# Kernel optimization log

Measured on AMD Instinct MI355X. Metric: run time of the kernel, lower is better.

Reference implementation:

```python
import jax, jax.numpy as jnp
import numpy as np

B, TP, TF = 256, 128, 64
COV, D, OUT, CTRL, H, L = 64, 64, 32, 128, 512, 2


def _gru_layer(x, Wih, Whh, bih, bhh):
    # x: [B, T, in]; torch GRU gate order: r, z, n
    xg = jnp.einsum('bti,gi->btg', x, Wih) + bih  # [B, T, 3H]
    h0 = jnp.zeros((x.shape[0], Whh.shape[1]), x.dtype)

    def step(h, xg_t):
        gh = h @ Whh.T + bhh
        xr, xz, xn = jnp.split(xg_t, 3, axis=-1)
        hr, hz, hn = jnp.split(gh, 3, axis=-1)
        r = jax.nn.sigmoid(xr + hr)
        z = jax.nn.sigmoid(xz + hz)
        n = jnp.tanh(xn + r * hn)
        h = (1.0 - z) * n + z * h
        return h, h

    _, hs = jax.lax.scan(step, h0, jnp.swapaxes(xg, 0, 1))
    return jnp.swapaxes(hs, 0, 1)  # [B, T, H]


def setup_inputs() -> dict:
    key = jax.random.key(0)
    ks = jax.random.split(key, 32)
    s = 0.05
    inp = {
        'past_input': jax.random.normal(ks[0], (B, TP, COV), jnp.float32),
        'past_label': jax.random.normal(ks[1], (B, TP, OUT), jnp.float32),
        'future_input': jax.random.normal(ks[2], (B, TF, COV), jnp.float32),
        'gru_Wih_0': s * jax.random.normal(ks[3], (3 * H, COV), jnp.float32),
        'gru_Whh_0': s * jax.random.normal(ks[4], (3 * H, H), jnp.float32),
        'gru_bih_0': s * jax.random.normal(ks[5], (3 * H,), jnp.float32),
        'gru_bhh_0': s * jax.random.normal(ks[6], (3 * H,), jnp.float32),
        'gru_Wih_1': s * jax.random.normal(ks[7], (3 * H, H), jnp.float32),
        'gru_Whh_1': s * jax.random.normal(ks[8], (3 * H, H), jnp.float32),
        'gru_bih_1': s * jax.random.normal(ks[9], (3 * H,), jnp.float32),
        'gru_bhh_1': s * jax.random.normal(ks[10], (3 * H,), jnp.float32),
        'flow_u': s * jax.random.normal(ks[11], (D,), jnp.float32),
        'flow_w': s * jax.random.normal(ks[12], (D,), jnp.float32),
        'flow_b': s * jax.random.normal(ks[13], (D,), jnp.float32),
        'feat_W': s * jax.random.normal(ks[14], (D, H), jnp.float32),
        'feat_b': s * jax.random.normal(ks[15], (D,), jnp.float32),
        'ctrl_W1': s * jax.random.normal(ks[16], (CTRL, OUT), jnp.float32),
        'ctrl_b1': s * jax.random.normal(ks[17], (CTRL,), jnp.float32),
        'ctrl_W2': s * jax.random.normal(ks[18], (2 * D, CTRL), jnp.float32),
        'ctrl_b2': s * jax.random.normal(ks[19], (2 * D,), jnp.float32),
        'ctrlmu_W': s * jax.random.normal(ks[20], (D, D), jnp.float32),
        'ctrlmu_b': s * jax.random.normal(ks[21], (D,), jnp.float32),
        'out_W': s * jax.random.normal(ks[22], (OUT, D), jnp.float32),
        'out_b': s * jax.random.normal(ks[23], (OUT,), jnp.float32),
    }
    return inp


def reference(past_input, past_label, future_input,
              gru_Wih_0, gru_Whh_0, gru_bih_0, gru_bhh_0,
              gru_Wih_1, gru_Whh_1, gru_bih_1, gru_bhh_1,
              flow_u, flow_w, flow_b, feat_W, feat_b,
              ctrl_W1, ctrl_b1, ctrl_W2, ctrl_b2,
              ctrlmu_W, ctrlmu_b, out_W, out_b):
    cov = jnp.concatenate([past_input, future_input], axis=1)  # [B, T, COV]
    h1 = _gru_layer(cov, gru_Wih_0, gru_Whh_0, gru_bih_0, gru_bhh_0)
    cov_feat = _gru_layer(h1, gru_Wih_1, gru_Whh_1, gru_bih_1, gru_bhh_1)  # [B, T, H]
    Tp = past_input.shape[1]
    bsz = past_input.shape[0]

    def trans(mu_past, var_past, cov_t):
        # per-dim PlanarFlow vectorized over transition_dim
        a = jnp.tanh(flow_w * mu_past + flow_b)
        mu_prior = flow_u * a + cov_t @ feat_W.T + feat_b + mu_past
        coef = flow_u * flow_w * (1.0 - a * a)
        var_prior = 2.0 * coef * var_past + var_past + 1.0
        return mu_prior, var_prior

    def control(ctrl_in, mu_prior):
        hdn = jnp.tanh(ctrl_in @ ctrl_W1.T + ctrl_b1)
        cm, cls = jnp.split(hdn @ ctrl_W2.T + ctrl_b2, 2, axis=-1)
        cm = cm - (mu_prior @ ctrlmu_W.T + ctrlmu_b)
        return cm, jax.nn.softplus(cls)

    def fuse(mu_pr, var_pr, mu_po, var_po):
        s = var_po + var_pr
        mu_w = (var_po / s) * mu_pr + (var_pr / s) * mu_po
        return mu_w, var_pr * var_po / s

    def past_step(carry, xs):
        mu_post, var_post = carry
        cov_t, lab_t = xs
        mu_pr, var_pr = trans(mu_post, var_post, cov_t)
        pred = mu_pr @ out_W.T + out_b
        cm, cs = control(lab_t, mu_pr)
        return fuse(mu_pr, var_pr, cm, cs), (pred, cm, cs)

    def fut_step(carry, cov_t):
        mu_post, var_post = carry
        mu_pr, var_pr = trans(mu_post, var_post, cov_t)
        pred = mu_pr @ out_W.T + out_b
        cm, cs = control(pred, mu_pr)
        return fuse(mu_pr, var_pr, cm, cs), (pred, cm, cs)

    init = (jnp.zeros((bsz, D), cov.dtype), jnp.ones((bsz, D), cov.dtype))
    cov_p = jnp.swapaxes(cov_feat[:, :Tp], 0, 1)
    lab_p = jnp.swapaxes(past_label, 0, 1)
    carry, (pp, cmp_, csp) = jax.lax.scan(past_step, init, (cov_p, lab_p))
    cov_f = jnp.swapaxes(cov_feat[:, Tp:], 0, 1)
    _, (pf, cmf, csf) = jax.lax.scan(fut_step, carry, cov_f)

    pred = jnp.swapaxes(jnp.concatenate([pp, pf], axis=0), 0, 1)        # [B, T, OUT]
    cm = jnp.swapaxes(jnp.concatenate([cmp_, cmf], axis=0), 0, 1)[:, 1:]  # [B, T-1, D]
    cs = jnp.swapaxes(jnp.concatenate([csp, csf], axis=0), 0, 1)[:, 1:]   # [B, T-1, D]
    return pred, cm, cs
```

## Files before the change

kernel.cpp:

```cpp
#include <hip/hip_runtime.h>
#include <stdint.h>

#define DEV static __device__ __forceinline__

using short8 = __attribute__((ext_vector_type(8))) short;
using f32x4  = __attribute__((ext_vector_type(4))) float;
using gbl_u32 = const __attribute__((address_space(1))) unsigned int;
using lds_u32 = __attribute__((address_space(3))) unsigned int;

DEV float bf2f(short s) {
  unsigned u = ((unsigned)(unsigned short)s) << 16;
  float f; __builtin_memcpy(&f, &u, 4); return f;
}
DEV short f2bf(float f) {
  unsigned u; __builtin_memcpy(&u, &f, 4);
  u = (u + 0x7fffu + ((u >> 16) & 1u)) >> 16;
  return (short)u;
}
DEV void gload_lds16(const void* g, void* l) {
  __builtin_amdgcn_global_load_lds((gbl_u32*)g, (lds_u32*)l, 16, 0, 0);
}
DEV float sigm(float x) { return 1.f / (1.f + __expf(-x)); }
DEV float tanh_f(float x) {
  float e = __expf(2.f * x);
  return 1.f - 2.f * __builtin_amdgcn_rcpf(e + 1.f);
}
DEV void bar() {
  asm volatile("s_waitcnt lgkmcnt(0)" ::: "memory");
  __builtin_amdgcn_sched_barrier(0);
  __builtin_amdgcn_s_barrier();
  __builtin_amdgcn_sched_barrier(0);
}

__global__ void pack_cov_k(const float* __restrict__ past, const float* __restrict__ fut,
                           short* __restrict__ covp) {
  const int n = 192 * 256 * 64;
  for (int i = blockIdx.x * blockDim.x + threadIdx.x; i < n; i += gridDim.x * blockDim.x) {
    int c = i & 63, r = i >> 6;
    int b = r & 255, t = r >> 8;
    float v = (t < 128) ? past[((size_t)b * 128 + t) * 64 + c]
                        : fut[((size_t)b * 64 + (t - 128)) * 64 + c];
    covp[i] = f2bf(v);
  }
}

__global__ void pack_lab_k(const float* __restrict__ lab, short* __restrict__ labp) {
  const int n = 128 * 256 * 32;
  for (int i = blockIdx.x * blockDim.x + threadIdx.x; i < n; i += gridDim.x * blockDim.x) {
    int c = i & 31, r = i >> 5;
    int b = r & 255, t = r >> 8;
    labp[i] = f2bf(lab[((size_t)b * 128 + t) * 32 + c]);
  }
}

DEV int gru_srcrow(int pr) {
  int j = pr / 96, w = pr % 96;
  return ((w >> 5) << 9) + j * 32 + (w & 31);
}

__global__ void pack_gru_k(const float* __restrict__ Wih, const float* __restrict__ Whh,
                           const float* __restrict__ bih, const float* __restrict__ bhh,
                           int Kin, short* __restrict__ Wihp, short* __restrict__ Whhp,
                           float* __restrict__ bihp, float* __restrict__ bhhp) {
  const int nW1 = 1536 * Kin, nW2 = 1536 * 512;
  const int total = nW1 + nW2 + 3072;
  for (int idx = blockIdx.x * blockDim.x + threadIdx.x; idx < total; idx += gridDim.x * blockDim.x) {
    if (idx < nW1) {
      int pr = idx / Kin, k = idx - pr * Kin;
      Wihp[idx] = f2bf(Wih[(size_t)gru_srcrow(pr) * Kin + k]);
    } else if (idx < nW1 + nW2) {
      int ii = idx - nW1;
      int j = ii / 49152, r = ii - j * 49152;
      int i = r & 7, slot = r >> 3;
      int l = slot & 63, sf = slot >> 6;
      int kqg = sf / 6, tile = sf - kqg * 6;
      int w = tile * 16 + (l & 15);
      int k = kqg * 32 + (l >> 4) * 8 + i;
      int srow = (w >> 5) * 512 + j * 32 + (w & 31);
      Whhp[ii] = f2bf(Whh[(size_t)srow * 512 + k]);
    } else if (idx < nW1 + nW2 + 1536) {
      int pr = idx - nW1 - nW2;
      bihp[pr] = bih[gru_srcrow(pr)];
    } else {
      int pr = idx - nW1 - nW2 - 1536;
      bhhp[pr] = bhh[gru_srcrow(pr)];
    }
  }
}

__global__ void pack_misc_k(const float* __restrict__ fw, const float* __restrict__ w1,
                            const float* __restrict__ w2, short* __restrict__ fwb,
                            short* __restrict__ w1b, short* __restrict__ w2b) {
  const int n1 = 64 * 512, n2 = 128 * 32, n3 = 128 * 128;
  const int total = n1 + n2 + n3;
  for (int i = blockIdx.x * blockDim.x + threadIdx.x; i < total; i += gridDim.x * blockDim.x) {
    if (i < n1) fwb[i] = f2bf(fw[i]);
    else if (i < n1 + n2) w1b[i - n1] = f2bf(w1[i - n1]);
    else w2b[i - n1 - n2] = f2bf(w2[i - n1 - n2]);
  }
}

__global__ void pack_vae_k(const float* __restrict__ outW, const float* __restrict__ cmuW,
                           const float* __restrict__ W1, const float* __restrict__ W2,
                           short* __restrict__ vwf) {
  const int n = 52 * 512;
  for (int i = blockIdx.x * blockDim.x + threadIdx.x; i < n; i += gridDim.x * blockDim.x) {
    int fr = i >> 9, l = (i >> 3) & 63, e = i & 7;
    int lm = l & 15, lh = l >> 4;
    float v;
    if (fr < 4) { int kt = fr >> 1, nt = fr & 1; v = outW[(nt * 16 + lm) * 64 + kt * 32 + lh * 8 + e]; }
    else if (fr < 12) { int f = fr - 4, kt = f >> 2, nt = f & 3; v = cmuW[(nt * 16 + lm) * 64 + kt * 32 + lh * 8 + e]; }
    else if (fr < 20) { int nt = fr - 12; v = W1[(nt * 16 + lm) * 32 + lh * 8 + e]; }
    else { int f = fr - 20, kt = f >> 3, nt = f & 7; v = W2[(nt * 16 + lm) * 128 + kt * 32 + lh * 8 + e]; }
    vwf[i] = f2bf(v);
  }
}

template <int BK, bool OBF16, bool DOTANH, bool AFRAG, int CMODE = 0>
__global__ __launch_bounds__(256) void gemm_bt_k(
    const short* __restrict__ A, const short* __restrict__ Bw,
    const float* __restrict__ bias, void* __restrict__ Cout,
    int M, int N, int K) {
  constexpr int BM = 128, BN = 128;
  __shared__ short As[BM * BK];
  __shared__ short Bs[BN * BK];
  const int tid = threadIdx.x, lane = tid & 63;
  const int wave = tid >> 6, wm = wave >> 1, wn = wave & 1;
  const int bm = blockIdx.x, bn = blockIdx.y;
  const int lm = lane & 15, lk = (lane >> 4) * 8;
  f32x4 acc[4][4] = {};
  for (int k0 = 0; k0 < K; k0 += BK) {
    constexpr int BYTES = BM * BK * 2;
#pragma unroll
    for (int it = 0; it < BYTES / 4096; ++it) {
      int o = it * 4096 + tid * 16;
      if (AFRAG) {
        int sub = o >> 10, gl = sub >> 1, kk2 = sub & 1, inb = o & 1023;
        size_t region = ((size_t)(bm >> 1) * 16 + (bm & 1) * 8 + gl) * 16 + (k0 >> 5) + kk2;
        gload_lds16((const char*)A + region * 1024 + inb, (char*)As + (o - lane * 16));
      } else {
        int row = o / (BK * 2);
        int col = o - row * (BK * 2);
        const char* srcA = (const char*)A + (((size_t)(bm * BM + row)) * K + k0) * 2 + col;
        gload_lds16(srcA, (char*)As + (o - lane * 16));
      }
      int row = o / (BK * 2);
      int col = o - row * (BK * 2);
      int rb = bn * BN + row;
      if (rb >= N) rb = N - 1;
      const char* srcB = (const char*)Bw + (((size_t)rb) * K + k0) * 2 + col;
      gload_lds16(srcB, (char*)Bs + (o - lane * 16));
    }
    __syncthreads();
#pragma unroll
    for (int kk = 0; kk < BK / 32; ++kk) {
      short8 av[4], bv[4];
#pragma unroll
      for (int i = 0; i < 4; ++i) {
        if (AFRAG)
          av[i] = *(const short8*)((const char*)As + (((wm * 4 + i) * 2 + kk) << 10) + lane * 16);
        else
          av[i] = *(const short8*)((const char*)As + ((wm * 64 + i * 16 + lm) * BK + kk * 32 + lk) * 2);
      }
#pragma unroll
      for (int jv = 0; jv < 4; ++jv)
        bv[jv] = *(const short8*)((const char*)Bs + ((wn * 64 + jv * 16 + lm) * BK + kk * 32 + lk) * 2);
#pragma unroll
      for (int i = 0; i < 4; ++i)
#pragma unroll
        for (int jv = 0; jv < 4; ++jv)
          acc[i][jv] = __builtin_amdgcn_mfma_f32_16x16x32_bf16(av[i], bv[jv], acc[i][jv], 0, 0, 0);
    }
    __syncthreads();
  }
  if (CMODE == 1) {
    const int NT = N >> 4;
#pragma unroll
    for (int jv = 0; jv < 4; ++jv) {
      int col = bn * BN + wn * 64 + jv * 16 + lm;
      if (col >= N) continue;
      float bvl = bias[col];
#pragma unroll
      for (int i = 0; i < 4; ++i) {
        int rowblk = bm * 8 + wm * 4 + i;
        f32x4 v = acc[i][jv];
        v[0] += bvl; v[1] += bvl; v[2] += bvl; v[3] += bvl;
        *(f32x4*)((float*)Cout + (((size_t)rowblk * NT + (col >> 4)) << 8) + lane * 4) = v;
      }
    }
  } else {
#pragma unroll
    for (int jv = 0; jv < 4; ++jv) {
      int col = bn * BN + wn * 64 + jv * 16 + lm;
      if (col >= N) continue;
      float bvl = bias[col];
#pragma unroll
      for (int i = 0; i < 4; ++i) {
        int row0 = bm * BM + wm * 64 + i * 16 + (lane >> 4) * 4;
#pragma unroll
        for (int r = 0; r < 4; ++r) {
          float v = acc[i][jv][r] + bvl;
          if (DOTANH) v = tanhf(v);
          size_t off = (size_t)(row0 + r) * N + col;
          if (OBF16) ((short*)Cout)[off] = f2bf(v);
          else ((float*)Cout)[off] = v;
        }
      }
    }
  }
}

template <int SCHEME>
__global__ __launch_bounds__(256) void gru_scan_k(
    const short* __restrict__ xg, const short* __restrict__ Whhp,
    const float* __restrict__ bhhp, short* __restrict__ hbuf,
    unsigned int* __restrict__ ctr, unsigned int* __restrict__ flags, int t0) {
  __shared__ short Wl[96 * 512];
  __shared__ short hs[16 * 512];
  __shared__ float sc[2][16 * 101];
  __shared__ float bhs[96];
  const int tid = threadIdx.x, lane = tid & 63, wave = tid >> 6;
  const int x = blockIdx.x;
  const int g = (x & 7) + ((x >> 7) << 3);
  const int j = (x >> 3) & 15;
  unsigned int* __restrict__ myctr = ctr + g * 64;
  unsigned int* __restrict__ myflags = flags + g * 16;
  unsigned int* __restrict__ hbuf32 = (unsigned int*)hbuf;
  {
    const char* wsrc = (const char*)Whhp + (size_t)j * 98304;
#pragma unroll 4
    for (int it = 0; it < 24; ++it) {
      int o = it * 4096 + tid * 16;
      gload_lds16(wsrc + o, (char*)Wl + (o - lane * 16));
    }
    if (tid < 96) bhs[tid] = bhhp[j * 96 + tid];
  }
  const int wk = wave >> 1, wn3 = wave & 1;
  const int m = tid >> 4, up = tid & 15, u0 = up * 2;
  for (int tl = 0; tl < 48; ++tl) {
    const int t = t0 + tl;
    const char* hsrc = (const char*)hbuf + ((size_t)t * 16 + g) * 16384;
#pragma unroll
    for (int it = 0; it < 4; ++it) {
      int o = it * 4096 + tid * 16;
      gload_lds16(hsrc + o, (char*)hs + (o - lane * 16));
    }
    const unsigned int* xp = (const unsigned int*)(xg + ((size_t)tl * 256 + g * 16 + m) * 1536 + j * 96);
    unsigned int xr2 = xp[up], xz2 = xp[16 + up], xn2 = xp[32 + up];
    __syncthreads();
    f32x4 a3[3] = {};
#pragma unroll
    for (int kq = 0; kq < 8; ++kq) {
      int kqg = wk * 8 + kq;
      short8 av = *(const short8*)((const char*)hs + (kqg << 10) + lane * 16);
#pragma unroll
      for (int n = 0; n < 3; ++n) {
        short8 bv = *(const short8*)((const char*)Wl + ((kqg * 6 + wn3 * 3 + n) << 10) + lane * 16);
        a3[n] = __builtin_amdgcn_mfma_f32_16x16x32_bf16(av, bv, a3[n], 0, 0, 0);
      }
    }
#pragma unroll
    for (int n = 0; n < 3; ++n)
#pragma unroll
      for (int rr = 0; rr < 4; ++rr)
        sc[wk][((lane >> 4) * 4 + rr) * 101 + (wn3 * 3 + n) * 16 + (lane & 15)] = a3[n][rr];
    __syncthreads();
    {
      float Sr0 = sc[0][m * 101 + u0] + sc[1][m * 101 + u0];
      float Sr1 = sc[0][m * 101 + u0 + 1] + sc[1][m * 101 + u0 + 1];
      float Sz0 = sc[0][m * 101 + 32 + u0] + sc[1][m * 101 + 32 + u0];
      float Sz1 = sc[0][m * 101 + 33 + u0] + sc[1][m * 101 + 33 + u0];
      float Sn0 = sc[0][m * 101 + 64 + u0] + sc[1][m * 101 + 64 + u0];
      float Sn1 = sc[0][m * 101 + 65 + u0] + sc[1][m * 101 + 65 + u0];
      int hpa = ((j * 64 + (up >> 2) * 16 + m) << 4) + ((u0 & 7) << 1);
      unsigned int hpu = *(const unsigned int*)((const char*)hs + hpa);
      float hp0 = bf2f((short)(hpu & 0xffff)), hp1 = bf2f((short)(hpu >> 16));
      float r0 = sigm(bf2f((short)(xr2 & 0xffff)) + Sr0 + bhs[u0]);
      float r1 = sigm(bf2f((short)(xr2 >> 16)) + Sr1 + bhs[u0 + 1]);
      float z0 = sigm(bf2f((short)(xz2 & 0xffff)) + Sz0 + bhs[32 + u0]);
      float z1 = sigm(bf2f((short)(xz2 >> 16)) + Sz1 + bhs[33 + u0]);
      float n0 = tanhf(bf2f((short)(xn2 & 0xffff)) + r0 * (Sn0 + bhs[64 + u0]));
      float n1 = tanhf(bf2f((short)(xn2 >> 16)) + r1 * (Sn1 + bhs[65 + u0]));
      float h0 = (1.f - z0) * n0 + z0 * hp0;
      float h1 = (1.f - z1) * n1 + z1 * hp1;
      unsigned int hv = (unsigned int)(unsigned short)f2bf(h0) |
                        ((unsigned int)(unsigned short)f2bf(h1) << 16);
      size_t oi = ((size_t)(t + 1) * 16 + g) * 4096 +
                  (j * 64 + (up >> 2) * 16 + m) * 4 + (up & 3);
      __hip_atomic_store(hbuf32 + oi, hv, __ATOMIC_RELAXED, __HIP_MEMORY_SCOPE_AGENT);
    }
    __syncthreads();
    if constexpr (SCHEME == 1) {
      if (tid == 0) {
        __hip_atomic_fetch_add(myctr, 1u, __ATOMIC_RELAXED, __HIP_MEMORY_SCOPE_AGENT);
        const unsigned tgt = 16u * (unsigned)(tl + 1);
        int guard = 0;
        while (__hip_atomic_load(myctr, __ATOMIC_RELAXED, __HIP_MEMORY_SCOPE_AGENT) < tgt &&
               ++guard < 200000) {}
      }
    } else {
      const unsigned tgt = (unsigned)(tl + 1);
      if (tid == 0)
        __hip_atomic_store(myflags + j, tgt, __ATOMIC_RELAXED, __HIP_MEMORY_SCOPE_AGENT);
      if (tid < 16) {
        int guard = 0;
        while (__hip_atomic_load(myflags + tid, __ATOMIC_RELAXED, __HIP_MEMORY_SCOPE_AGENT) < tgt &&
               ++guard < 200000) {}
      }
    }
    __syncthreads();
  }
}

#define PAST_STEP(T, FN, CMR, CSR)                                           \
  do {                                                                       \
    f32x4 muPr, varPr;                                                       \
    _Pragma("unroll") for (int r = 0; r < 4; ++r) {                          \
      float m_ = muC[r];                                                     \
      float a_ = tanh_f(fw1 * m_ + fb1);                                     \
      muPr[r] = fu1 * a_ + FN[r] + m_;                                       \
      float cf_ = fu1 * fw1 * (1.f - a_ * a_);                               \
      varPr[r] = 2.f * cf_ * varC[r] + varC[r] + 1.f;                        \
    }                                                                        \
    f32x4 cmNow = CMR, csNow = CSR;                                          \
    FN = *(const f32x4*)(feat_img + (((size_t)((T) + 2) * 16 + bg) * 4 + w) * 256 + l * 4); \
    if ((T) + 2 < 128) {                                                     \
      CMR = *(const f32x4*)(ctrl_img + (((size_t)((T) + 2) * 16 + bg) * 8 + w) * 256 + l * 4); \
      CSR = *(const f32x4*)(ctrl_img + (((size_t)((T) + 2) * 16 + bg) * 8 + 4 + w) * 256 + l * 4); \
    }                                                                        \
    _Pragma("unroll") for (int r = 0; r < 4; ++r) {                          \
      int row_ = m4 * 4 + r;                                                 \
      *(short*)((char*)muA + ((row_ * 128 + (w * 16 + c) * 2) ^ ((row_ & 7) << 4))) = f2bf(muPr[r]); \
    }                                                                        \
    bar();                                                                   \
    short8 muAf0 = *(const short8*)((const char*)muA + ((c * 128 + m4 * 16) ^ ((c & 7) << 4))); \
    short8 muAf1 = *(const short8*)((const char*)muA + ((c * 128 + 64 + m4 * 16) ^ ((c & 7) << 4))); \
    if (w == 0) *(short8*)(muprb + (((size_t)(T) * 16 + bg) * 2) * 512 + l * 8) = muAf0; \
    if (w == 1) *(short8*)(muprb + (((size_t)(T) * 16 + bg) * 2 + 1) * 512 + l * 8) = muAf1; \
    f32x4 mcC = {0.f, 0.f, 0.f, 0.f};                                        \
    mcC = __builtin_amdgcn_mfma_f32_16x16x32_bf16(muAf0, cmuf0, mcC, 0, 0, 0); \
    mcC = __builtin_amdgcn_mfma_f32_16x16x32_bf16(muAf1, cmuf1, mcC, 0, 0, 0); \
    bar();                                                                   \
    _Pragma("unroll") for (int r = 0; r < 4; ++r) {                          \
      float vp_ = varPr[r], mp_ = muPr[r];                                   \
      float cmv_ = cmNow[r] - (mcC[r] + cmub1);                              \
      float x_ = csNow[r];                                                   \
      float cs_ = (x_ > 20.f) ? x_ : __logf(1.f + __expf(x_));               \
      if ((T) >= 1) {                                                        \
        size_t b_ = (size_t)(bg * 16 + m4 * 4 + r);                          \
        out[1572864 + b_ * 12224 + (size_t)((T) - 1) * 64 + w * 16 + c] = cmv_; \
        out[4702208 + b_ * 12224 + (size_t)((T) - 1) * 64 + w * 16 + c] = cs_;  \
      }                                                                      \
      float s_ = cs_ + vp_;                                                  \
      float rs_ = __builtin_amdgcn_rcpf(s_);                                 \
      muC[r] = cs_ * rs_ * mp_ + vp_ * rs_ * cmv_;                           \
      varC[r] = vp_ * cs_ * rs_;                                             \
    }                                                                        \
  } while (0)

#define FUT_STEP(T, FN)                                                      \
  do {                                                                       \
    f32x4 muPr, varPr;                                                       \
    _Pragma("unroll") for (int r = 0; r < 4; ++r) {                          \
      float m_ = muC[r];                                                     \
      float a_ = tanh_f(fw1 * m_ + fb1);                                     \
      muPr[r] = fu1 * a_ + FN[r] + m_;                                       \
      float cf_ = fu1 * fw1 * (1.f - a_ * a_);                               \
      varPr[r] = 2.f * cf_ * varC[r] + varC[r] + 1.f;                        \
    }                                                                        \
    if ((T) + 2 < 192)                                                       \
      FN = *(const f32x4*)(feat_img + (((size_t)((T) + 2) * 16 + bg) * 4 + w) * 256 + l * 4); \
    _Pragma("unroll") for (int r = 0; r < 4; ++r) {                          \
      int row_ = m4 * 4 + r;                                                 \
      *(short*)((char*)muA + ((row_ * 128 + (w * 16 + c) * 2) ^ ((row_ & 7) << 4))) = f2bf(muPr[r]); \
    }                                                                        \
    bar();                                                                   \
    short8 muAf0 = *(const short8*)((const char*)muA + ((c * 128 + m4 * 16) ^ ((c & 7) << 4))); \
    short8 muAf1 = *(const short8*)((const char*)muA + ((c * 128 + 64 + m4 * 16) ^ ((c & 7) << 4))); \
    f32x4 mcC = {0.f, 0.f, 0.f, 0.f};                                        \
    mcC = __builtin_amdgcn_mfma_f32_16x16x32_bf16(muAf0, cmuf0, mcC, 0, 0, 0); \
    mcC = __builtin_amdgcn_mfma_f32_16x16x32_bf16(muAf1, cmuf1, mcC, 0, 0, 0); \
    if (w < 2) {                                                             \
      f32x4 predC = {0.f, 0.f, 0.f, 0.f};                                    \
      predC = __builtin_amdgcn_mfma_f32_16x16x32_bf16(muAf0, outWf0, predC, 0, 0, 0); \
      predC = __builtin_amdgcn_mfma_f32_16x16x32_bf16(muAf1, outWf1, predC, 0, 0, 0); \
      _Pragma("unroll") for (int r = 0; r < 4; ++r) {                        \
        float pv_ = predC[r] + outb1;                                        \
        out[(size_t)(bg * 16 + m4 * 4 + r) * 6144 + (T) * 32 + w * 16 + c] = pv_; \
        int row_ = m4 * 4 + r;                                               \
        *(short*)((char*)predA + ((row_ * 64 + (w * 16 + c) * 2) ^ ((row_ & 3) << 4))) = f2bf(pv_); \
      }                                                                      \
    }                                                                        \
    bar();                                                                   \
    short8 pAf = *(const short8*)((const char*)predA + ((c * 64 + m4 * 16) ^ ((c & 3) << 4))); \
    f32x4 z0 = {0.f, 0.f, 0.f, 0.f}, z1 = {0.f, 0.f, 0.f, 0.f};              \
    z0 = __builtin_amdgcn_mfma_f32_16x16x32_bf16(pAf, *(const short8*)((const char*)Wctl + (2 * w) * 1024 + l * 16), z0, 0, 0, 0); \
    z1 = __builtin_amdgcn_mfma_f32_16x16x32_bf16(pAf, *(const short8*)((const char*)Wctl + (2 * w + 1) * 1024 + l * 16), z1, 0, 0, 0); \
    _Pragma("unroll") for (int r = 0; r < 4; ++r) {                          \
      int row_ = m4 * 4 + r;                                                 \
      *(short*)((char*)hdnA + ((row_ * 256 + ((2 * w) * 16 + c) * 2) ^ ((row_ & 7) << 4))) = f2bf(tanh_f(z0[r] + b1a)); \
      *(short*)((char*)hdnA + ((row_ * 256 + ((2 * w + 1) * 16 + c) * 2) ^ ((row_ & 7) << 4))) = f2bf(tanh_f(z1[r] + b1b)); \
    }                                                                        \
    bar();                                                                   \
    short8 hAf0 = *(const short8*)((const char*)hdnA + ((c * 256 + 0 * 64 + m4 * 16) ^ ((c & 7) << 4))); \
    short8 hAf1 = *(const short8*)((const char*)hdnA + ((c * 256 + 1 * 64 + m4 * 16) ^ ((c & 7) << 4))); \
    short8 hAf2 = *(const short8*)((const char*)hdnA + ((c * 256 + 2 * 64 + m4 * 16) ^ ((c & 7) << 4))); \
    short8 hAf3 = *(const short8*)((const char*)hdnA + ((c * 256 + 3 * 64 + m4 * 16) ^ ((c & 7) << 4))); \
    f32x4 zcm = {0.f, 0.f, 0.f, 0.f}, zcs = {0.f, 0.f, 0.f, 0.f};            \
    zcm = __builtin_amdgcn_mfma_f32_16x16x32_bf16(hAf0, *(const short8*)((const char*)Wctl + (8 + 0 * 8 + w) * 1024 + l * 16), zcm, 0, 0, 0); \
    zcm = __builtin_amdgcn_mfma_f32_16x16x32_bf16(hAf1, *(const short8*)((const char*)Wctl + (8 + 1 * 8 + w) * 1024 + l * 16), zcm, 0, 0, 0); \
    zcm = __builtin_amdgcn_mfma_f32_16x16x32_bf16(hAf2, *(const short8*)((const char*)Wctl + (8 + 2 * 8 + w) * 1024 + l * 16), zcm, 0, 0, 0); \
    zcm = __builtin_amdgcn_mfma_f32_16x16x32_bf16(hAf3, *(const short8*)((const char*)Wctl + (8 + 3 * 8 + w) * 1024 + l * 16), zcm, 0, 0, 0); \
    zcs = __builtin_amdgcn_mfma_f32_16x16x32_bf16(hAf0, *(const short8*)((const char*)Wctl + (8 + 0 * 8 + 4 + w) * 1024 + l * 16), zcs, 0, 0, 0); \
    zcs = __builtin_amdgcn_mfma_f32_16x16x32_bf16(hAf1, *(const short8*)((const char*)Wctl + (8 + 1 * 8 + 4 + w) * 1024 + l * 16), zcs, 0, 0, 0); \
    zcs = __builtin_amdgcn_mfma_f32_16x16x32_bf16(hAf2, *(const short8*)((const char*)Wctl + (8 + 2 * 8 + 4 + w) * 1024 + l * 16), zcs, 0, 0, 0); \
    zcs = __builtin_amdgcn_mfma_f32_16x16x32_bf16(hAf3, *(const short8*)((const char*)Wctl + (8 + 3 * 8 + 4 + w) * 1024 + l * 16), zcs, 0, 0, 0); \
    bar();                                                                   \
    _Pragma("unroll") for (int r = 0; r < 4; ++r) {                          \
      float vp_ = varPr[r], mp_ = muPr[r];                                   \
      float cmv_ = (zcm[r] + b2cm) - (mcC[r] + cmub1);                       \
      float x_ = zcs[r] + b2cs;                                              \
      float cs_ = (x_ > 20.f) ? x_ : __logf(1.f + __expf(x_));               \
      size_t b_ = (size_t)(bg * 16 + m4 * 4 + r);                            \
      out[1572864 + b_ * 12224 + (size_t)((T) - 1) * 64 + w * 16 + c] = cmv_; \
      out[4702208 + b_ * 12224 + (size_t)((T) - 1) * 64 + w * 16 + c] = cs_;  \
      float s_ = cs_ + vp_;                                                  \
      float rs_ = __builtin_amdgcn_rcpf(s_);                                 \
      muC[r] = cs_ * rs_ * mp_ + vp_ * rs_ * cmv_;                           \
      varC[r] = vp_ * cs_ * rs_;                                             \
    }                                                                        \
  } while (0)

__global__ __launch_bounds__(256) void vae_k(
    const float* __restrict__ feat_img, const float* __restrict__ ctrl_img,
    const short* __restrict__ vwf,
    const float* __restrict__ flow_u, const float* __restrict__ flow_w,
    const float* __restrict__ flow_b, const float* __restrict__ outb,
    const float* __restrict__ b1, const float* __restrict__ b2,
    const float* __restrict__ cmub, short* __restrict__ muprb,
    float* __restrict__ out) {
  __shared__ short Wctl[40 * 512];
  __shared__ short muA[16 * 64];
  __shared__ short predA[16 * 32];
  __shared__ short hdnA[16 * 128];
  const int tid = threadIdx.x, l = tid & 63, w = tid >> 6;
  const int m4 = l >> 4, c = l & 15, bg = blockIdx.x;
  {
    const char* src = (const char*)vwf + 12288;
#pragma unroll
    for (int it = 0; it < 10; ++it) {
      int o = it * 4096 + tid * 16;
      gload_lds16(src + o, (char*)Wctl + (o - l * 16));
    }
  }
  short8 cmuf0 = *(const short8*)(vwf + (4 + w) * 512 + l * 8);
  short8 cmuf1 = *(const short8*)(vwf + (8 + w) * 512 + l * 8);
  short8 outWf0 = *(const short8*)(vwf + ((w & 1)) * 512 + l * 8);
  short8 outWf1 = *(const short8*)(vwf + (2 + (w & 1)) * 512 + l * 8);
  float fw1 = flow_w[w * 16 + c], fu1 = flow_u[w * 16 + c];
  float fb1 = flow_b[w * 16 + c], cmub1 = cmub[w * 16 + c];
  float outb1 = outb[(w & 1) * 16 + c];
  float b1a = b1[(2 * w) * 16 + c], b1b = b1[(2 * w + 1) * 16 + c];
  float b2cm = b2[w * 16 + c], b2cs = b2[(4 + w) * 16 + c];
  f32x4 muC = {0.f, 0.f, 0.f, 0.f}, varC = {1.f, 1.f, 1.f, 1.f};
  f32x4 fN0 = *(const f32x4*)(feat_img + ((size_t)bg * 4 + w) * 256 + l * 4);
  f32x4 fN1 = *(const f32x4*)(feat_img + ((size_t)(16 + bg) * 4 + w) * 256 + l * 4);
  f32x4 cmA = *(const f32x4*)(ctrl_img + ((size_t)bg * 8 + w) * 256 + l * 4);
  f32x4 csA = *(const f32x4*)(ctrl_img + ((size_t)bg * 8 + 4 + w) * 256 + l * 4);
  f32x4 cmB = *(const f32x4*)(ctrl_img + ((size_t)(16 + bg) * 8 + w) * 256 + l * 4);
  f32x4 csB = *(const f32x4*)(ctrl_img + ((size_t)(16 + bg) * 8 + 4 + w) * 256 + l * 4);
  __syncthreads();
  for (int t2 = 0; t2 < 128; t2 += 2) {
    PAST_STEP(t2, fN0, cmA, csA);
    PAST_STEP(t2 + 1, fN1, cmB, csB);
  }
  asm volatile("s_waitcnt vmcnt(0)" ::: "memory");
  __builtin_amdgcn_sched_barrier(0);
  __builtin_amdgcn_s_barrier();
  for (int t2 = 128; t2 < 192; t2 += 2) {
    FUT_STEP(t2, fN0);
    FUT_STEP(t2 + 1, fN1);
  }
}

__global__ __launch_bounds__(512) void pred_past_k(
    const short* __restrict__ muprb, const short* __restrict__ vwf,
    const float* __restrict__ outb, float* __restrict__ out) {
  const int l = threadIdx.x & 63;
  const int w = blockIdx.x * 8 + (threadIdx.x >> 6);
  const int t = w >> 4, bg = w & 15;
  const int m4 = l >> 4, c = l & 15;
  short8 a0 = *(const short8*)(muprb + ((size_t)w * 2 + 0) * 512 + l * 8);
  short8 a1 = *(const short8*)(muprb + ((size_t)w * 2 + 1) * 512 + l * 8);
  float outb2[2] = {outb[c], outb[16 + c]};
#pragma unroll
  for (int nt = 0; nt < 2; ++nt) {
    short8 w0 = *(const short8*)(vwf + (0 * 2 + nt) * 512 + l * 8);
    short8 w1 = *(const short8*)(vwf + (1 * 2 + nt) * 512 + l * 8);
    f32x4 p = {0.f, 0.f, 0.f, 0.f};
    p = __builtin_amdgcn_mfma_f32_16x16x32_bf16(a0, w0, p, 0, 0, 0);
    p = __builtin_amdgcn_mfma_f32_16x16x32_bf16(a1, w1, p, 0, 0, 0);
#pragma unroll
    for (int r = 0; r < 4; ++r)
      out[(size_t)(bg * 16 + m4 * 4 + r) * 6144 + t * 32 + nt * 16 + c] = p[r] + outb2[nt];
  }
}

extern "C" void kernel_launch(void* const* d_in, const int* in_sizes, int n_in,
                              void* d_out, int out_size, void* d_ws, size_t ws_size,
                              hipStream_t stream) {
  (void)in_sizes; (void)n_in; (void)out_size; (void)ws_size;
  const float* past_input = (const float*)d_in[0];
  const float* past_label = (const float*)d_in[1];
  const float* future_input = (const float*)d_in[2];
  const float* Wih0 = (const float*)d_in[3];
  const float* Whh0 = (const float*)d_in[4];
  const float* bih0 = (const float*)d_in[5];
  const float* bhh0 = (const float*)d_in[6];
  const float* Wih1 = (const float*)d_in[7];
  const float* Whh1 = (const float*)d_in[8];
  const float* bih1 = (const float*)d_in[9];
  const float* bhh1 = (const float*)d_in[10];
  const float* flow_u = (const float*)d_in[11];
  const float* flow_w = (const float*)d_in[12];
  const float* flow_b = (const float*)d_in[13];
  const float* feat_W = (const float*)d_in[14];
  const float* feat_b = (const float*)d_in[15];
  const float* ctrl_W1 = (const float*)d_in[16];
  const float* ctrl_b1 = (const float*)d_in[17];
  const float* ctrl_W2 = (const float*)d_in[18];
  const float* ctrl_b2 = (const float*)d_in[19];
  const float* cmuW = (const float*)d_in[20];
  const float* cmub = (const float*)d_in[21];
  const float* outW = (const float*)d_in[22];
  const float* outb = (const float*)d_in[23];

  char* ws = (char*)d_ws;
  size_t off = 0;
  auto alloc = [&](size_t bytes) -> char* {
    char* p = ws + off;
    off += (bytes + 255) & ~(size_t)255;
    return p;
  };
  short* covp  = (short*)alloc(49152ull * 64 * 2);
  short* labp  = (short*)alloc(32768ull * 32 * 2);
  short* Wih0p = (short*)alloc(1536ull * 64 * 2);
  short* Whh0p = (short*)alloc(1536ull * 512 * 2);
  short* Wih1p = (short*)alloc(1536ull * 512 * 2);
  short* Whh1p = (short*)alloc(1536ull * 512 * 2);
  float* bih0p = (float*)alloc(1536 * 4);
  float* bhh0p = (float*)alloc(1536 * 4);
  float* bih1p = (float*)alloc(1536 * 4);
  float* bhh1p = (float*)alloc(1536 * 4);
  short* featWb = (short*)alloc(64ull * 512 * 2);
  short* W1b   = (short*)alloc(128ull * 32 * 2);
  short* W2b   = (short*)alloc(128ull * 128 * 2);
  short* vwf   = (short*)alloc(52ull * 512 * 2);
  short* xgc   = (short*)alloc(48ull * 256 * 1536 * 2);
  short* h1buf = (short*)alloc(193ull * 256 * 512 * 2);
  short* cfbuf = (short*)alloc(193ull * 256 * 512 * 2);
  unsigned int* ctr = (unsigned int*)alloc(8 * 16 * 64 * 4);
  unsigned int* flg = (unsigned int*)alloc(8 * 16 * 16 * 4);
  float* feat_img = (float*)xgc;
  short* hdnb     = (short*)((char*)xgc + 12582912);
  float* ctrl_img = (float*)((char*)xgc + 20971520);
  short* muprb    = (short*)covp;

  hipMemsetAsync(ctr, 0, 8 * 16 * 64 * 4, stream);
  hipMemsetAsync(flg, 0, 8 * 16 * 16 * 4, stream);
  hipMemsetAsync(h1buf, 0, 256 * 512 * 2, stream);
  hipMemsetAsync(cfbuf, 0, 256 * 512 * 2, stream);

  pack_cov_k<<<2048, 256, 0, stream>>>(past_input, future_input, covp);
  pack_lab_k<<<1024, 256, 0, stream>>>(past_label, labp);
  pack_gru_k<<<1024, 256, 0, stream>>>(Wih0, Whh0, bih0, bhh0, 64, Wih0p, Whh0p, bih0p, bhh0p);
  pack_gru_k<<<1024, 256, 0, stream>>>(Wih1, Whh1, bih1, bhh1, 512, Wih1p, Whh1p, bih1p, bhh1p);
  pack_misc_k<<<64, 256, 0, stream>>>(feat_W, ctrl_W1, ctrl_W2, featWb, W1b, W2b);
  pack_vae_k<<<104, 256, 0, stream>>>(outW, cmuW, ctrl_W1, ctrl_W2, vwf);

  for (int c = 0; c < 4; ++c) {
    gemm_bt_k<64, true, false, false><<<dim3(96, 12), 256, 0, stream>>>(
        covp + (size_t)c * 48 * 256 * 64, Wih0p, bih0p, xgc, 12288, 1536, 64);
    int d = c;
    if (c & 1)
      gru_scan_k<2><<<256, 256, 0, stream>>>(xgc, Whh0p, bhh0p, h1buf,
                                             ctr + d * 1024, flg + d * 256, c * 48);
    else
      gru_scan_k<1><<<256, 256, 0, stream>>>(xgc, Whh0p, bhh0p, h1buf,
                                             ctr + d * 1024, flg + d * 256, c * 48);
  }
  for (int c = 0; c < 4; ++c) {
    gemm_bt_k<64, true, false, true><<<dim3(96, 12), 256, 0, stream>>>(
        h1buf + (size_t)(1 + c * 48) * 131072, Wih1p, bih1p, xgc, 12288, 1536, 512);
    int d = 4 + c;
    if (c & 1)
      gru_scan_k<2><<<256, 256, 0, stream>>>(xgc, Whh1p, bhh1p, cfbuf,
                                             ctr + d * 1024, flg + d * 256, c * 48);
    else
      gru_scan_k<1><<<256, 256, 0, stream>>>(xgc, Whh1p, bhh1p, cfbuf,
                                             ctr + d * 1024, flg + d * 256, c * 48);
  }
  gemm_bt_k<64, false, false, true, 1><<<dim3(384, 1), 256, 0, stream>>>(
      cfbuf + 131072, featWb, feat_b, feat_img, 49152, 64, 512);
  gemm_bt_k<32, true, true, false><<<dim3(256, 1), 256, 0, stream>>>(
      labp, W1b, ctrl_b1, hdnb, 32768, 128, 32);
  gemm_bt_k<64, false, false, false, 1><<<dim3(256, 1), 256, 0, stream>>>(
      hdnb, W2b, ctrl_b2, ctrl_img, 32768, 128, 128);

  vae_k<<<16, 256, 0, stream>>>(feat_img, ctrl_img, vwf, flow_u, flow_w, flow_b,
                                outb, ctrl_b1, ctrl_b2, cmub, muprb, (float*)d_out);
  pred_past_k<<<256, 512, 0, stream>>>(muprb, vwf, outb, (float*)d_out);
}
```

Baseline: 1.389 ms.

## Fuse layer-0 input projection into GRU scan and run all 192 steps in one launch

The layer-0 GRU input projection (K=64) is now computed inside the recurrent scan kernel with extra MFMAs on pre-packed covariate and Wih0 fragments. This removes the separate chunked GEMMs, the xg round trip through global memory, and three kernel launches for layer 0. The r/z input biases are folded into the hidden biases, and the n-gate input part is kept separate so the reset gate applies only to the hidden term. The spin-wait also now polls with an sc0 global load before the agent-scope atomic load. The trade-off is added MFMA and LDS work on the serial critical path of every step.

```diff
diff --git a/kernel.cpp b/kernel.cpp
--- a/kernel.cpp
+++ b/kernel.cpp
@@ -24,6 +24,15 @@
 DEV float tanh_f(float x) {
   float e = __expf(2.f * x);
   return 1.f - 2.f * __builtin_amdgcn_rcpf(e + 1.f);
+}
+DEV unsigned load_sc0(const unsigned int* p) {
+  unsigned v;
+  asm volatile("global_load_dword %0, %1, off sc0\n\ts_waitcnt vmcnt(0)"
+               : "=v"(v) : "v"(p) : "memory");
+  return v;
+}
+DEV unsigned load_agent(const unsigned int* p) {
+  return __hip_atomic_load(p, __ATOMIC_RELAXED, __HIP_MEMORY_SCOPE_AGENT);
 }
 DEV void bar() {
   asm volatile("s_waitcnt lgkmcnt(0)" ::: "memory");
@@ -32,15 +41,16 @@
   __builtin_amdgcn_sched_barrier(0);
 }
 
-__global__ void pack_cov_k(const float* __restrict__ past, const float* __restrict__ fut,
-                           short* __restrict__ covp) {
-  const int n = 192 * 256 * 64;
+__global__ void pack_covf_k(const float* __restrict__ past, const float* __restrict__ fut,
+                            short* __restrict__ covf) {
+  const int n = 192 * 16 * 2 * 512;
   for (int i = blockIdx.x * blockDim.x + threadIdx.x; i < n; i += gridDim.x * blockDim.x) {
-    int c = i & 63, r = i >> 6;
-    int b = r & 255, t = r >> 8;
-    float v = (t < 128) ? past[((size_t)b * 128 + t) * 64 + c]
-                        : fut[((size_t)b * 64 + (t - 128)) * 64 + c];
-    covp[i] = f2bf(v);
+    int e = i & 7, l = (i >> 3) & 63, kf = (i >> 9) & 1, g = (i >> 10) & 15, t = i >> 14;
+    int b = g * 16 + (l & 15);
+    int col = kf * 32 + (l >> 4) * 8 + e;
+    float v = (t < 128) ? past[((size_t)b * 128 + t) * 64 + col]
+                        : fut[((size_t)b * 64 + (t - 128)) * 64 + col];
+    covf[i] = f2bf(v);
   }
 }
 
@@ -88,6 +98,17 @@
   }
 }
 
+__global__ void pack_wih0f_k(const float* __restrict__ Wih0, short* __restrict__ wf) {
+  const int n = 16 * 6 * 2 * 512;
+  for (int i = blockIdx.x * blockDim.x + threadIdx.x; i < n; i += gridDim.x * blockDim.x) {
+    int j = i / 6144, r = i - j * 6144;
+    int tile = r >> 10, kf = (r >> 9) & 1, l = (r >> 3) & 63, e = r & 7;
+    int srow = gru_srcrow(j * 96 + tile * 16 + (l & 15));
+    int k = kf * 32 + (l >> 4) * 8 + e;
+    wf[i] = f2bf(Wih0[(size_t)srow * 64 + k]);
+  }
+}
+
 __global__ void pack_misc_k(const float* __restrict__ fw, const float* __restrict__ w1,
                             const float* __restrict__ w2, short* __restrict__ fwb,
                             short* __restrict__ w1b, short* __restrict__ w2b) {
@@ -210,15 +231,24 @@
   }
 }
 
-template <int SCHEME>
+template <int SCHEME, int XGF>
 __global__ __launch_bounds__(256) void gru_scan_k(
-    const short* __restrict__ xg, const short* __restrict__ Whhp,
-    const float* __restrict__ bhhp, short* __restrict__ hbuf,
-    unsigned int* __restrict__ ctr, unsigned int* __restrict__ flags, int t0) {
+    const short* __restrict__ xg,
+    const short* __restrict__ covf,
+    const short* __restrict__ wihf_g,
+    const short* __restrict__ Whhp,
+    const float* __restrict__ bihp,
+    const float* __restrict__ bhhp,
+    short* __restrict__ hbuf,
+    unsigned int* __restrict__ ctr,
+    unsigned int* __restrict__ flags,
+    int t0, int nsteps) {
   __shared__ short Wl[96 * 512];
   __shared__ short hs[16 * 512];
   __shared__ float sc[2][16 * 101];
+  __shared__ float scx[2][16 * 33];
   __shared__ float bhs[96];
+  __shared__ float bihn[32];
   const int tid = threadIdx.x, lane = tid & 63, wave = tid >> 6;
   const int x = blockIdx.x;
   const int g = (x & 7) + ((x >> 7) << 3);
@@ -233,11 +263,22 @@
       int o = it * 4096 + tid * 16;
       gload_lds16(wsrc + o, (char*)Wl + (o - lane * 16));
     }
-    if (tid < 96) bhs[tid] = bhhp[j * 96 + tid];
+    if (tid < 96) {
+      float b = bhhp[j * 96 + tid];
+      if (XGF && tid < 64) b += bihp[j * 96 + tid];
+      bhs[tid] = b;
+    }
+    if (XGF && tid < 32) bihn[tid] = bihp[j * 96 + 64 + tid];
   }
   const int wk = wave >> 1, wn3 = wave & 1;
   const int m = tid >> 4, up = tid & 15, u0 = up * 2;
-  for (int tl = 0; tl < 48; ++tl) {
+  short8 wihf0{}, wihf1{}, wihf2{};
+  if (XGF) {
+    wihf0 = *(const short8*)(wihf_g + ((size_t)(j * 6 + wn3 * 3 + 0) * 2 + wk) * 512 + lane * 8);
+    wihf1 = *(const short8*)(wihf_g + ((size_t)(j * 6 + wn3 * 3 + 1) * 2 + wk) * 512 + lane * 8);
+    wihf2 = *(const short8*)(wihf_g + ((size_t)(j * 6 + wn3 * 3 + 2) * 2 + wk) * 512 + lane * 8);
+  }
+  for (int tl = 0; tl < nsteps; ++tl) {
     const int t = t0 + tl;
     const char* hsrc = (const char*)hbuf + ((size_t)t * 16 + g) * 16384;
 #pragma unroll
@@ -245,10 +286,17 @@
       int o = it * 4096 + tid * 16;
       gload_lds16(hsrc + o, (char*)hs + (o - lane * 16));
     }
-    const unsigned int* xp = (const unsigned int*)(xg + ((size_t)tl * 256 + g * 16 + m) * 1536 + j * 96);
-    unsigned int xr2 = xp[up], xz2 = xp[16 + up], xn2 = xp[32 + up];
+    short8 cf{};
+    unsigned int xr2 = 0, xz2 = 0, xn2 = 0;
+    if (XGF) {
+      cf = *(const short8*)(covf + (((size_t)t * 16 + g) * 2 + wk) * 512 + lane * 8);
+    } else {
+      const unsigned int* xp = (const unsigned int*)(xg + ((size_t)tl * 256 + g * 16 + m) * 1536 + j * 96);
+      xr2 = xp[up]; xz2 = xp[16 + up]; xn2 = xp[32 + up];
+    }
     __syncthreads();
     f32x4 a3[3] = {};
+    f32x4 ax0 = {0.f, 0.f, 0.f, 0.f}, ax1 = {0.f, 0.f, 0.f, 0.f};
 #pragma unroll
     for (int kq = 0; kq < 8; ++kq) {
       int kqg = wk * 8 + kq;
@@ -259,11 +307,28 @@
         a3[n] = __builtin_amdgcn_mfma_f32_16x16x32_bf16(av, bv, a3[n], 0, 0, 0);
       }
     }
+    if (XGF) {
+      a3[0] = __builtin_amdgcn_mfma_f32_16x16x32_bf16(cf, wihf0, a3[0], 0, 0, 0);
+      if (wn3 == 0) {
+        a3[1] = __builtin_amdgcn_mfma_f32_16x16x32_bf16(cf, wihf1, a3[1], 0, 0, 0);
+        a3[2] = __builtin_amdgcn_mfma_f32_16x16x32_bf16(cf, wihf2, a3[2], 0, 0, 0);
+      } else {
+        ax0 = __builtin_amdgcn_mfma_f32_16x16x32_bf16(cf, wihf1, ax0, 0, 0, 0);
+        ax1 = __builtin_amdgcn_mfma_f32_16x16x32_bf16(cf, wihf2, ax1, 0, 0, 0);
+      }
+    }
 #pragma unroll
     for (int n = 0; n < 3; ++n)
 #pragma unroll
       for (int rr = 0; rr < 4; ++rr)
         sc[wk][((lane >> 4) * 4 + rr) * 101 + (wn3 * 3 + n) * 16 + (lane & 15)] = a3[n][rr];
+    if (XGF && wn3 == 1) {
+#pragma unroll
+      for (int rr = 0; rr < 4; ++rr) {
+        scx[wk][((lane >> 4) * 4 + rr) * 33 + (lane & 15)] = ax0[rr];
+        scx[wk][((lane >> 4) * 4 + rr) * 33 + 16 + (lane & 15)] = ax1[rr];
+      }
+    }
     __syncthreads();
     {
       float Sr0 = sc[0][m * 101 + u0] + sc[1][m * 101 + u0];
@@ -275,12 +340,24 @@
       int hpa = ((j * 64 + (up >> 2) * 16 + m) << 4) + ((u0 & 7) << 1);
       unsigned int hpu = *(const unsigned int*)((const char*)hs + hpa);
       float hp0 = bf2f((short)(hpu & 0xffff)), hp1 = bf2f((short)(hpu >> 16));
-      float r0 = sigm(bf2f((short)(xr2 & 0xffff)) + Sr0 + bhs[u0]);
-      float r1 = sigm(bf2f((short)(xr2 >> 16)) + Sr1 + bhs[u0 + 1]);
-      float z0 = sigm(bf2f((short)(xz2 & 0xffff)) + Sz0 + bhs[32 + u0]);
-      float z1 = sigm(bf2f((short)(xz2 >> 16)) + Sz1 + bhs[33 + u0]);
-      float n0 = tanhf(bf2f((short)(xn2 & 0xffff)) + r0 * (Sn0 + bhs[64 + u0]));
-      float n1 = tanhf(bf2f((short)(xn2 >> 16)) + r1 * (Sn1 + bhs[65 + u0]));
+      float r0, r1, z0, z1, n0, n1;
+      if (XGF) {
+        float Sx0 = scx[0][m * 33 + u0] + scx[1][m * 33 + u0];
+        float Sx1 = scx[0][m * 33 + u0 + 1] + scx[1][m * 33 + u0 + 1];
+        r0 = sigm(Sr0 + bhs[u0]);
+        r1 = sigm(Sr1 + bhs[u0 + 1]);
+        z0 = sigm(Sz0 + bhs[32 + u0]);
+        z1 = sigm(Sz1 + bhs[33 + u0]);
+        n0 = tanhf(Sx0 + bihn[u0] + r0 * (Sn0 + bhs[64 + u0]));
+        n1 = tanhf(Sx1 + bihn[u0 + 1] + r1 * (Sn1 + bhs[65 + u0]));
+      } else {
+        r0 = sigm(bf2f((short)(xr2 & 0xffff)) + Sr0 + bhs[u0]);
+        r1 = sigm(bf2f((short)(xr2 >> 16)) + Sr1 + bhs[u0 + 1]);
+        z0 = sigm(bf2f((short)(xz2 & 0xffff)) + Sz0 + bhs[32 + u0]);
+        z1 = sigm(bf2f((short)(xz2 >> 16)) + Sz1 + bhs[33 + u0]);
+        n0 = tanhf(bf2f((short)(xn2 & 0xffff)) + r0 * (Sn0 + bhs[64 + u0]));
+        n1 = tanhf(bf2f((short)(xn2 >> 16)) + r1 * (Sn1 + bhs[65 + u0]));
+      }
       float h0 = (1.f - z0) * n0 + z0 * hp0;
       float h1 = (1.f - z1) * n1 + z1 * hp1;
       unsigned int hv = (unsigned int)(unsigned short)f2bf(h0) |
@@ -295,8 +372,11 @@
         __hip_atomic_fetch_add(myctr, 1u, __ATOMIC_RELAXED, __HIP_MEMORY_SCOPE_AGENT);
         const unsigned tgt = 16u * (unsigned)(tl + 1);
         int guard = 0;
-        while (__hip_atomic_load(myctr, __ATOMIC_RELAXED, __HIP_MEMORY_SCOPE_AGENT) < tgt &&
-               ++guard < 200000) {}
+        for (;;) {
+          if (load_sc0(myctr) >= tgt) break;
+          if (load_agent(myctr) >= tgt) break;
+          if (++guard >= 200000) break;
+        }
       }
     } else {
       const unsigned tgt = (unsigned)(tl + 1);
@@ -304,8 +384,11 @@
         __hip_atomic_store(myflags + j, tgt, __ATOMIC_RELAXED, __HIP_MEMORY_SCOPE_AGENT);
       if (tid < 16) {
         int guard = 0;
-        while (__hip_atomic_load(myflags + tid, __ATOMIC_RELAXED, __HIP_MEMORY_SCOPE_AGENT) < tgt &&
-               ++guard < 200000) {}
+        for (;;) {
+          if (load_sc0(myflags + tid) >= tgt) break;
+          if (load_agent(myflags + tid) >= tgt) break;
+          if (++guard >= 200000) break;
+        }
       }
     }
     __syncthreads();
@@ -542,7 +625,7 @@
     off += (bytes + 255) & ~(size_t)255;
     return p;
   };
-  short* covp  = (short*)alloc(49152ull * 64 * 2);
+  short* covf  = (short*)alloc(192ull * 16 * 2 * 512 * 2);
   short* labp  = (short*)alloc(32768ull * 32 * 2);
   short* Wih0p = (short*)alloc(1536ull * 64 * 2);
   short* Whh0p = (short*)alloc(1536ull * 512 * 2);
@@ -556,6 +639,7 @@
   short* W1b   = (short*)alloc(128ull * 32 * 2);
   short* W2b   = (short*)alloc(128ull * 128 * 2);
   short* vwf   = (short*)alloc(52ull * 512 * 2);
+  short* wih0f = (short*)alloc(16ull * 6 * 2 * 512 * 2);
   short* xgc   = (short*)alloc(48ull * 256 * 1536 * 2);
   short* h1buf = (short*)alloc(193ull * 256 * 512 * 2);
   short* cfbuf = (short*)alloc(193ull * 256 * 512 * 2);
@@ -564,41 +648,36 @@
   float* feat_img = (float*)xgc;
   short* hdnb     = (short*)((char*)xgc + 12582912);
   float* ctrl_img = (float*)((char*)xgc + 20971520);
-  short* muprb    = (short*)covp;
+  short* muprb    = (short*)covf;
 
   hipMemsetAsync(ctr, 0, 8 * 16 * 64 * 4, stream);
   hipMemsetAsync(flg, 0, 8 * 16 * 16 * 4, stream);
   hipMemsetAsync(h1buf, 0, 256 * 512 * 2, stream);
   hipMemsetAsync(cfbuf, 0, 256 * 512 * 2, stream);
 
-  pack_cov_k<<<2048, 256, 0, stream>>>(past_input, future_input, covp);
+  pack_covf_k<<<2048, 256, 0, stream>>>(past_input, future_input, covf);
   pack_lab_k<<<1024, 256, 0, stream>>>(past_label, labp);
   pack_gru_k<<<1024, 256, 0, stream>>>(Wih0, Whh0, bih0, bhh0, 64, Wih0p, Whh0p, bih0p, bhh0p);
   pack_gru_k<<<1024, 256, 0, stream>>>(Wih1, Whh1, bih1, bhh1, 512, Wih1p, Whh1p, bih1p, bhh1p);
+  pack_wih0f_k<<<96, 256, 0, stream>>>(Wih0, wih0f);
   pack_misc_k<<<64, 256, 0, stream>>>(feat_W, ctrl_W1, ctrl_W2, featWb, W1b, W2b);
   pack_vae_k<<<104, 256, 0, stream>>>(outW, cmuW, ctrl_W1, ctrl_W2, vwf);
 
-  for (int c = 0; c < 4; ++c) {
-    gemm_bt_k<64, true, false, false><<<dim3(96, 12), 256, 0, stream>>>(
-        covp + (size_t)c * 48 * 256 * 64, Wih0p, bih0p, xgc, 12288, 1536, 64);
-    int d = c;
-    if (c & 1)
-      gru_scan_k<2><<<256, 256, 0, stream>>>(xgc, Whh0p, bhh0p, h1buf,
-                                             ctr + d * 1024, flg + d * 256, c * 48);
-    else
-      gru_scan_k<1><<<256, 256, 0, stream>>>(xgc, Whh0p, bhh0p, h1buf,
-                                             ctr + d * 1024, flg + d * 256, c * 48);
-  }
+  gru_scan_k<2, 1><<<256, 256, 0, stream>>>(
+      nullptr, covf, wih0f, Whh0p, bih0p, bhh0p, h1buf,
+      ctr, flg, 0, 192);
   for (int c = 0; c < 4; ++c) {
     gemm_bt_k<64, true, false, true><<<dim3(96, 12), 256, 0, stream>>>(
         h1buf + (size_t)(1 + c * 48) * 131072, Wih1p, bih1p, xgc, 12288, 1536, 512);
     int d = 4 + c;
     if (c & 1)
-      gru_scan_k<2><<<256, 256, 0, stream>>>(xgc, Whh1p, bhh1p, cfbuf,
-                                             ctr + d * 1024, flg + d * 256, c * 48);
+      gru_scan_k<2, 0><<<256, 256, 0, stream>>>(
+          xgc, nullptr, nullptr, Whh1p, nullptr, bhh1p, cfbuf,
+          ctr + d * 1024, flg + d * 256, c * 48, 48);
     else
-      gru_scan_k<1><<<256, 256, 0, stream>>>(xgc, Whh1p, bhh1p, cfbuf,
-                                             ctr + d * 1024, flg + d * 256, c * 48);
+      gru_scan_k<1, 0><<<256, 256, 0, stream>>>(
+          xgc, nullptr, nullptr, Whh1p, nullptr, bhh1p, cfbuf,
+          ctr + d * 1024, flg + d * 256, c * 48, 48);
   }
   gemm_bt_k<64, false, false, true, 1><<<dim3(384, 1), 256, 0, stream>>>(
       cfbuf + 131072, featWb, feat_b, feat_img, 49152, 64, 512);
```

Measured after the change: 1.349 ms. 2.9% less time.
